# Kernel optimization log

Hardware: AMD Instinct MI355X
Metric: run time of the kernel (lower is better)

## Reference

```python
import jax, jax.numpy as jnp
import numpy as np

N = 100000
E = 1600000
D_IN = 128
D_OUT = 128
BN_EPS = 1e-5


def setup_inputs() -> dict:
    key = jax.random.key(0)
    k = jax.random.split(key, 8)
    feats = jax.random.normal(k[0], (N, D_IN), dtype=jnp.float32)
    src = jax.random.randint(k[1], (E,), 0, N, dtype=jnp.int32)
    dst = jax.random.randint(k[2], (E,), 0, N, dtype=jnp.int32)
    # GraphConv weight (in, out) + bias, residual Linear, batchnorm affine
    W = jax.random.normal(k[3], (D_IN, D_OUT), dtype=jnp.float32) / np.sqrt(D_IN)
    b = jnp.zeros((D_OUT,), dtype=jnp.float32)
    Wr = jax.random.normal(k[4], (D_IN, D_OUT), dtype=jnp.float32) / np.sqrt(D_IN)
    br = jnp.zeros((D_OUT,), dtype=jnp.float32)
    gamma = jnp.ones((D_OUT,), dtype=jnp.float32)
    beta = jnp.zeros((D_OUT,), dtype=jnp.float32)
    return {"feats": feats, "src": src, "dst": dst, "W": W, "b": b,
            "Wr": Wr, "br": br, "gamma": gamma, "beta": beta}


def reference(feats, src, dst, W, b, Wr, br, gamma, beta):
    ones = jnp.ones((src.shape[0],), dtype=feats.dtype)
    out_deg = jax.ops.segment_sum(ones, src, num_segments=N)
    in_deg = jax.ops.segment_sum(ones, dst, num_segments=N)
    norm_src = jax.lax.rsqrt(jnp.maximum(out_deg, 1.0))  # [N]
    norm_dst = jax.lax.rsqrt(jnp.maximum(in_deg, 1.0))   # [N]

    # GraphConv, norm='both' (in_feats == out_feats -> aggregate then matmul)
    h = feats * norm_src[:, None]
    agg = jax.ops.segment_sum(h[src], dst, num_segments=N)  # [N, D_IN]
    agg = agg * norm_dst[:, None]
    conv = jax.nn.relu(agg @ W + b)

    # residual linear + activation
    res = jax.nn.relu(feats @ Wr + br)
    y = conv + res  # dropout p=0 -> identity

    # BatchNorm1d (batch statistics, biased variance)
    mean = jnp.mean(y, axis=0)
    var = jnp.var(y, axis=0)
    y = (y - mean) * jax.lax.rsqrt(var + BN_EPS) * gamma + beta
    return y
```

## Files before the change

kernel.cpp:

```cpp
#include <hip/hip_runtime.h>

#define NN 100000
#define DD 128
#define EE 1600000
#define BN_EPS 1e-5f
#define NBLK 3125
#define NCH 2
#define CH 50000
#define CW (CH / 4)
#define NEB 64
#define EPB (EE / NEB)

using bf16x8 = __attribute__((ext_vector_type(8))) short;
using f32x4  = __attribute__((ext_vector_type(4))) float;

__device__ __forceinline__ unsigned short bf16r(float f) {
    unsigned u = __float_as_uint(f);
    u += 0x7FFF + ((u >> 16) & 1);
    return (unsigned short)(u >> 16);
}
__device__ __forceinline__ float bf2f(unsigned short h) {
    return __uint_as_float((unsigned)h << 16);
}

__global__ __launch_bounds__(1024) void hist_kernel(
    const int4* __restrict__ src4, const int4* __restrict__ dst4,
    unsigned short* __restrict__ outT, unsigned short* __restrict__ inT,
    unsigned char* __restrict__ lrank) {
    __shared__ unsigned outc[CW];
    __shared__ unsigned inc[CW];
    const int j = blockIdx.x & (NEB - 1);
    const int c = blockIdx.x >> 6;
    const int clo = c * CH;
    const int t = threadIdx.x;
    for (int i = t; i < CW; i += 1024) { outc[i] = 0; inc[i] = 0; }
    __syncthreads();
    const int base = j * (EPB / 4);
    for (int i = t; i < EPB / 4; i += 1024) {
        int4 s = src4[base + i];
        int4 d = dst4[base + i];
        int e = j * EPB + i * 4;
        unsigned sx = (unsigned)(s.x - clo);
        unsigned sy = (unsigned)(s.y - clo);
        unsigned sz = (unsigned)(s.z - clo);
        unsigned sw = (unsigned)(s.w - clo);
        if (sx < CH) atomicAdd(&outc[sx >> 2], 1u << ((sx & 3) * 8));
        if (sy < CH) atomicAdd(&outc[sy >> 2], 1u << ((sy & 3) * 8));
        if (sz < CH) atomicAdd(&outc[sz >> 2], 1u << ((sz & 3) * 8));
        if (sw < CH) atomicAdd(&outc[sw >> 2], 1u << ((sw & 3) * 8));
        unsigned dx = (unsigned)(d.x - clo);
        unsigned dy = (unsigned)(d.y - clo);
        unsigned dz = (unsigned)(d.z - clo);
        unsigned dw = (unsigned)(d.w - clo);
        if (dx < CH) { unsigned o = atomicAdd(&inc[dx >> 2], 1u << ((dx & 3) * 8)); lrank[e + 0] = (unsigned char)(o >> ((dx & 3) * 8)); }
        if (dy < CH) { unsigned o = atomicAdd(&inc[dy >> 2], 1u << ((dy & 3) * 8)); lrank[e + 1] = (unsigned char)(o >> ((dy & 3) * 8)); }
        if (dz < CH) { unsigned o = atomicAdd(&inc[dz >> 2], 1u << ((dz & 3) * 8)); lrank[e + 2] = (unsigned char)(o >> ((dz & 3) * 8)); }
        if (dw < CH) { unsigned o = atomicAdd(&inc[dw >> 2], 1u << ((dw & 3) * 8)); lrank[e + 3] = (unsigned char)(o >> ((dw & 3) * 8)); }
    }
    __syncthreads();
    ushort4* op = (ushort4*)(outT + (size_t)j * NN + clo);
    ushort4* ip = (ushort4*)(inT + (size_t)j * NN + clo);
    for (int i = t; i < CW; i += 1024) {
        unsigned vo = outc[i], vi = inc[i];
        ushort4 ho, hi;
        ho.x = (unsigned short)(vo & 0xFFu);
        ho.y = (unsigned short)((vo >> 8) & 0xFFu);
        ho.z = (unsigned short)((vo >> 16) & 0xFFu);
        ho.w = (unsigned short)(vo >> 24);
        hi.x = (unsigned short)(vi & 0xFFu);
        hi.y = (unsigned short)((vi >> 8) & 0xFFu);
        hi.z = (unsigned short)((vi >> 16) & 0xFFu);
        hi.w = (unsigned short)(vi >> 24);
        op[i] = ho;
        ip[i] = hi;
    }
}

__global__ void degscan_kernel(const unsigned short* __restrict__ outT,
                               unsigned short* __restrict__ inT,
                               int* __restrict__ indeg, float* __restrict__ ns,
                               float* __restrict__ nd) {
    int n = blockIdx.x * blockDim.x + threadIdx.x;
    if (n < NN) {
        int run_in = 0, run_out = 0;
#pragma unroll 8
        for (int j = 0; j < NEB; ++j) {
            run_out += (int)outT[(size_t)j * NN + n];
            int ci = (int)inT[(size_t)j * NN + n];
            inT[(size_t)j * NN + n] = (unsigned short)run_in;
            run_in += ci;
        }
        indeg[n] = run_in;
        ns[n] = rsqrtf(fmaxf((float)run_out, 1.0f));
        nd[n] = rsqrtf(fmaxf((float)run_in, 1.0f));
    }
}

__global__ __launch_bounds__(1024) void scan1_kernel(const int* __restrict__ indeg,
                                                     int* __restrict__ partial,
                                                     int* __restrict__ blocksum) {
    __shared__ int s[1024];
    int t = threadIdx.x;
    int idx = blockIdx.x * 1024 + t;
    int v = (idx < NN) ? indeg[idx] : 0;
    s[t] = v;
    __syncthreads();
    for (int off = 1; off < 1024; off <<= 1) {
        int x = (t >= off) ? s[t - off] : 0;
        __syncthreads();
        s[t] += x;
        __syncthreads();
    }
    if (idx < NN) partial[idx] = s[t] - v;
    if (t == 1023) blocksum[blockIdx.x] = s[t];
}

__global__ void scan23_kernel(const int* __restrict__ partial, const int* __restrict__ blocksum,
                              int* __restrict__ row_ofs) {
    __shared__ int s[128];
    int t = threadIdx.x;
    if (t < 128) s[t] = (t < 98) ? blocksum[t] : 0;
    __syncthreads();
    for (int off = 1; off < 128; off <<= 1) {
        int x = (t < 128 && t >= off) ? s[t - off] : 0;
        __syncthreads();
        if (t < 128) s[t] += x;
        __syncthreads();
    }
    int i = blockIdx.x * blockDim.x + t;
    if (i < NN) {
        int bk = i >> 10;
        row_ofs[i] = partial[i] + s[bk] - blocksum[bk];
        if (i == 0) row_ofs[NN] = EE;
    }
}

__global__ void fill4_kernel(const int4* __restrict__ src4, const int4* __restrict__ dst4,
                             const unsigned short* __restrict__ baseT,
                             const uchar4* __restrict__ lrank4,
                             const int* __restrict__ row_ofs, int* __restrict__ e_src) {
    int i = blockIdx.x * blockDim.x + threadIdx.x;
    if (i < EE / 4) {
        int4 s = src4[i];
        int4 d = dst4[i];
        uchar4 r = lrank4[i];
        int j = (i * 4) / EPB;
        const unsigned short* bT = baseT + (size_t)j * NN;
        e_src[row_ofs[d.x] + (int)bT[d.x] + (int)r.x] = s.x;
        e_src[row_ofs[d.y] + (int)bT[d.y] + (int)r.y] = s.y;
        e_src[row_ofs[d.z] + (int)bT[d.z] + (int)r.z] = s.z;
        e_src[row_ofs[d.w] + (int)bT[d.w] + (int)r.w] = s.w;
    }
}

__global__ void cvt_kernel(const float4* __restrict__ feats4, const float* __restrict__ ns,
                           ushort4* __restrict__ fb4) {
    int i = blockIdx.x * blockDim.x + threadIdx.x;
    if (i < NN * 32) {
        float s = ns[i >> 5];
        float4 v = feats4[i];
        ushort4 h;
        h.x = bf16r(v.x * s);
        h.y = bf16r(v.y * s);
        h.z = bf16r(v.z * s);
        h.w = bf16r(v.w * s);
        fb4[i] = h;
    }
}

__global__ void prepw_kernel(const float* __restrict__ W, const float* __restrict__ Wr,
                             unsigned short* __restrict__ wb) {
    int g = blockIdx.x >> 5;
    int f = blockIdx.x & 31;
    int ct = f >> 2, ks = f & 3;
    int l = threadIdx.x;
    const float* G = g ? Wr : W;
    unsigned short* hi = wb + (((size_t)(g * 2 + 0) * 32 + f) * 64 + l) * 8;
    unsigned short* lo = wb + (((size_t)(g * 2 + 1) * 32 + f) * 64 + l) * 8;
    for (int i = 0; i < 8; ++i) {
        int k = ks * 32 + (l >> 4) * 8 + i;
        int col = ct * 16 + (l & 15);
        float w = G[k * 128 + col];
        unsigned uh = __float_as_uint(w) & 0xFFFF0000u;
        hi[i] = (unsigned short)(uh >> 16);
        lo[i] = bf16r(w - __uint_as_float(uh));
    }
}

__device__ __forceinline__ void accum8(float* a, int4 u) {
    a[0] += __uint_as_float((unsigned)u.x << 16);
    a[1] += __uint_as_float((unsigned)u.x & 0xFFFF0000u);
    a[2] += __uint_as_float((unsigned)u.y << 16);
    a[3] += __uint_as_float((unsigned)u.y & 0xFFFF0000u);
    a[4] += __uint_as_float((unsigned)u.z << 16);
    a[5] += __uint_as_float((unsigned)u.z & 0xFFFF0000u);
    a[6] += __uint_as_float((unsigned)u.w << 16);
    a[7] += __uint_as_float((unsigned)u.w & 0xFFFF0000u);
}

__global__ __launch_bounds__(256, 6) void gather_kernel(
    const int4* __restrict__ fbi, const float* __restrict__ nd,
    const int* __restrict__ row_ofs, const int* __restrict__ e_src,
    float* __restrict__ y) {
    const int lane = threadIdx.x & 15;
    const int grp = threadIdx.x >> 4;
    const int node = blockIdx.x * 16 + grp;
    const int beg = row_ofs[node];
    const int end = row_ofs[node + 1];

    float a0[8] = {0.f, 0.f, 0.f, 0.f, 0.f, 0.f, 0.f, 0.f};
    float a1[8] = {0.f, 0.f, 0.f, 0.f, 0.f, 0.f, 0.f, 0.f};

    for (int e = beg; e < end; e += 16) {
        int cnt = end - e;
        if (cnt > 16) cnt = 16;
        int myidx = (lane < cnt) ? e_src[e + lane] : 0;
        int j = 0;
        for (; j + 3 < cnt; j += 4) {
            int s0 = __shfl(myidx, j, 16);
            int s1 = __shfl(myidx, j + 1, 16);
            int s2 = __shfl(myidx, j + 2, 16);
            int s3 = __shfl(myidx, j + 3, 16);
            int4 u0 = fbi[(size_t)s0 * 16 + lane];
            int4 u1 = fbi[(size_t)s1 * 16 + lane];
            int4 u2 = fbi[(size_t)s2 * 16 + lane];
            int4 u3 = fbi[(size_t)s3 * 16 + lane];
            accum8(a0, u0);
            accum8(a1, u1);
            accum8(a0, u2);
            accum8(a1, u3);
        }
        for (; j < cnt; ++j) {
            int s0 = __shfl(myidx, j, 16);
            int4 u0 = fbi[(size_t)s0 * 16 + lane];
            accum8(a0, u0);
        }
    }

    float snd = nd[node];
    float4 o0, o1;
    o0.x = (a0[0] + a1[0]) * snd;
    o0.y = (a0[1] + a1[1]) * snd;
    o0.z = (a0[2] + a1[2]) * snd;
    o0.w = (a0[3] + a1[3]) * snd;
    o1.x = (a0[4] + a1[4]) * snd;
    o1.y = (a0[5] + a1[5]) * snd;
    o1.z = (a0[6] + a1[6]) * snd;
    o1.w = (a0[7] + a1[7]) * snd;
    ((float4*)y)[(size_t)node * 32 + lane * 2] = o0;
    ((float4*)y)[(size_t)node * 32 + lane * 2 + 1] = o1;
}

__device__ __forceinline__ void hilo4(float4 v, ushort4& h, ushort4& l) {
    unsigned u0 = __float_as_uint(v.x) & 0xFFFF0000u;
    unsigned u1 = __float_as_uint(v.y) & 0xFFFF0000u;
    unsigned u2 = __float_as_uint(v.z) & 0xFFFF0000u;
    unsigned u3 = __float_as_uint(v.w) & 0xFFFF0000u;
    h.x = (unsigned short)(u0 >> 16);
    h.y = (unsigned short)(u1 >> 16);
    h.z = (unsigned short)(u2 >> 16);
    h.w = (unsigned short)(u3 >> 16);
    l.x = bf16r(v.x - __uint_as_float(u0));
    l.y = bf16r(v.y - __uint_as_float(u1));
    l.z = bf16r(v.z - __uint_as_float(u2));
    l.w = bf16r(v.w - __uint_as_float(u3));
}

__global__ __launch_bounds__(256, 4) void gemm_kernel(
    const float4* __restrict__ feats4,
    const unsigned short* __restrict__ wb,
    const float* __restrict__ b, const float* __restrict__ br,
    float* y, float* __restrict__ part_sum, float* __restrict__ part_sq) {
    __shared__ unsigned short AsH[32 * 128];
    __shared__ unsigned short AsL[32 * 128];
    __shared__ unsigned short FsH[32 * 128];
    __shared__ unsigned short FsL[32 * 128];

    const int tid = threadIdx.x;
    const int block_row = blockIdx.x * 32;
    const float4* agg4 = (const float4*)y;

    for (int i = tid; i < 1024; i += 256) {
        int r = i >> 5;
        int c4 = i & 31;
        size_t g = (size_t)(block_row + r) * 32 + c4;
        float4 a = agg4[g];
        float4 f = feats4[g];
        int off = (r * 256 + ((c4 * 8) ^ ((r & 7) << 4))) >> 1;
        ushort4 h, l;
        hilo4(a, h, l);
        *(ushort4*)(&AsH[off]) = h;
        *(ushort4*)(&AsL[off]) = l;
        hilo4(f, h, l);
        *(ushort4*)(&FsH[off]) = h;
        *(ushort4*)(&FsL[off]) = l;
    }
    __syncthreads();

    const int w = tid >> 6;
    const int l = tid & 63;
    const int lr = l & 15;
    const int lh = l >> 4;
    const int ct0 = w * 2;
    const bf16x8* WB = (const bf16x8*)wb;

    const f32x4 fzero = {0.f, 0.f, 0.f, 0.f};
    f32x4 aC[2][2], aR[2][2];
#pragma unroll
    for (int r = 0; r < 2; ++r)
#pragma unroll
        for (int c = 0; c < 2; ++c) { aC[r][c] = fzero; aR[r][c] = fzero; }

#pragma unroll 1
    for (int ks = 0; ks < 4; ++ks) {
        bf16x8 ah[2], al[2], fh[2], fl[2];
#pragma unroll
        for (int r = 0; r < 2; ++r) {
            int row = r * 16 + lr;
            int off = (row * 256 + ((ks * 64 + lh * 16) ^ ((row & 7) << 4))) >> 1;
            ah[r] = *(const bf16x8*)(&AsH[off]);
            al[r] = *(const bf16x8*)(&AsL[off]);
            fh[r] = *(const bf16x8*)(&FsH[off]);
            fl[r] = *(const bf16x8*)(&FsL[off]);
        }
#pragma unroll
        for (int c = 0; c < 2; ++c) {
            int fr = (ct0 + c) * 4 + ks;
            bf16x8 wh  = WB[(0 * 32 + fr) * 64 + l];
            bf16x8 wl  = WB[(1 * 32 + fr) * 64 + l];
            bf16x8 wrh = WB[(2 * 32 + fr) * 64 + l];
            bf16x8 wrl = WB[(3 * 32 + fr) * 64 + l];
#pragma unroll
            for (int r = 0; r < 2; ++r) {
                aC[r][c] = __builtin_amdgcn_mfma_f32_16x16x32_bf16(ah[r], wh, aC[r][c], 0, 0, 0);
                aC[r][c] = __builtin_amdgcn_mfma_f32_16x16x32_bf16(al[r], wh, aC[r][c], 0, 0, 0);
                aC[r][c] = __builtin_amdgcn_mfma_f32_16x16x32_bf16(ah[r], wl, aC[r][c], 0, 0, 0);
                aR[r][c] = __builtin_amdgcn_mfma_f32_16x16x32_bf16(fh[r], wrh, aR[r][c], 0, 0, 0);
                aR[r][c] = __builtin_amdgcn_mfma_f32_16x16x32_bf16(fl[r], wrh, aR[r][c], 0, 0, 0);
                aR[r][c] = __builtin_amdgcn_mfma_f32_16x16x32_bf16(fh[r], wrl, aR[r][c], 0, 0, 0);
            }
        }
    }

#pragma unroll
    for (int c = 0; c < 2; ++c) {
        int col = (ct0 + c) * 16 + lr;
        float bv = b[col], brv = br[col];
        float cs = 0.f, cq = 0.f;
#pragma unroll
        for (int r = 0; r < 2; ++r) {
#pragma unroll
            for (int i = 0; i < 4; ++i) {
                float o = fmaxf(aC[r][c][i] + bv, 0.f) + fmaxf(aR[r][c][i] + brv, 0.f);
                int grow = block_row + r * 16 + lh * 4 + i;
                y[(size_t)grow * 128 + col] = o;
                cs += o;
                cq += o * o;
            }
        }
        cs += __shfl_xor(cs, 16); cs += __shfl_xor(cs, 32);
        cq += __shfl_xor(cq, 16); cq += __shfl_xor(cq, 32);
        if (lh == 0) {
            part_sum[(size_t)blockIdx.x * 128 + col] = cs;
            part_sq[(size_t)blockIdx.x * 128 + col] = cq;
        }
    }
}

__global__ __launch_bounds__(256) void colreduce_kernel(
    const float* __restrict__ part_sum, const float* __restrict__ part_sq,
    float* __restrict__ colsum, float* __restrict__ colsumsq) {
    int j = blockIdx.x;
    int t = threadIdx.x;
    float s = 0.f, q = 0.f;
    for (int bb = t; bb < NBLK; bb += 256) {
        s += part_sum[(size_t)bb * 128 + j];
        q += part_sq[(size_t)bb * 128 + j];
    }
#pragma unroll
    for (int off = 1; off < 64; off <<= 1) {
        s += __shfl_xor(s, off);
        q += __shfl_xor(q, off);
    }
    __shared__ float ss[4], qq[4];
    if ((t & 63) == 0) { ss[t >> 6] = s; qq[t >> 6] = q; }
    __syncthreads();
    if (t == 0) {
        colsum[j] = ss[0] + ss[1] + ss[2] + ss[3];
        colsumsq[j] = qq[0] + qq[1] + qq[2] + qq[3];
    }
}

__global__ void apply2_kernel(float4* __restrict__ y4,
                              const float* __restrict__ colsum, const float* __restrict__ colsumsq,
                              const float* __restrict__ gamma, const float* __restrict__ beta) {
    __shared__ float sc4[128], sh4[128];
    int t = threadIdx.x;
    if (t < 128) {
        const float inv_n = 1.0f / (float)NN;
        float mean = colsum[t] * inv_n;
        float var = colsumsq[t] * inv_n - mean * mean;
        float s = gamma[t] * rsqrtf(var + BN_EPS);
        sc4[t] = s;
        sh4[t] = beta[t] - mean * s;
    }
    __syncthreads();
    int i = blockIdx.x * 256 + t;
    if (i < NN * 32) {
        int c = (i & 31) * 4;
        float4 v = y4[i];
        v.x = v.x * sc4[c + 0] + sh4[c + 0];
        v.y = v.y * sc4[c + 1] + sh4[c + 1];
        v.z = v.z * sc4[c + 2] + sh4[c + 2];
        v.w = v.w * sc4[c + 3] + sh4[c + 3];
        y4[i] = v;
    }
}

extern "C" void kernel_launch(void* const* d_in, const int* in_sizes, int n_in,
                              void* d_out, int out_size, void* d_ws, size_t ws_size,
                              hipStream_t stream) {
    const float* feats = (const float*)d_in[0];
    const int* src = (const int*)d_in[1];
    const int* dst = (const int*)d_in[2];
    const float* W = (const float*)d_in[3];
    const float* b = (const float*)d_in[4];
    const float* Wr = (const float*)d_in[5];
    const float* br = (const float*)d_in[6];
    const float* gamma = (const float*)d_in[7];
    const float* beta = (const float*)d_in[8];
    float* y = (float*)d_out;

    char* ws = (char*)d_ws;
    unsigned short* outT = (unsigned short*)ws;
    unsigned short* inT = outT + (size_t)NEB * NN;
    unsigned char* lrank = (unsigned char*)(inT + (size_t)NEB * NN);
    ushort4* fb4 = (ushort4*)ws;
    float* part_sum = (float*)lrank;
    float* part_sq = part_sum + (size_t)NBLK * 128;
    char* wsB = ws + (size_t)2 * NEB * NN * 2 + (size_t)EE * 2;
    float* ns = (float*)wsB;
    float* nd = ns + NN;
    int* row_ofs = (int*)(nd + NN);
    int* indeg = row_ofs + NN + 1;
    int* partial = indeg + NN;
    int* blocksum = partial + NN;
    int* e_src = blocksum + 128;
    float* colsum = (float*)(e_src + EE);
    float* colsumsq = colsum + DD;
    unsigned long long wbofs = (unsigned long long)((char*)(colsumsq + DD) - ws);
    wbofs = (wbofs + 255ull) & ~255ull;
    unsigned short* wb = (unsigned short*)(ws + wbofs);

    prepw_kernel<<<64, 64, 0, stream>>>(W, Wr, wb);
    hist_kernel<<<NCH * NEB, 1024, 0, stream>>>((const int4*)src, (const int4*)dst,
                                                outT, inT, lrank);
    degscan_kernel<<<(NN + 255) / 256, 256, 0, stream>>>(outT, inT, indeg, ns, nd);
    scan1_kernel<<<98, 1024, 0, stream>>>(indeg, partial, blocksum);
    scan23_kernel<<<(NN + 255) / 256, 256, 0, stream>>>(partial, blocksum, row_ofs);
    fill4_kernel<<<(EE / 4 + 255) / 256, 256, 0, stream>>>((const int4*)src, (const int4*)dst,
                                                           inT, (const uchar4*)lrank,
                                                           row_ofs, e_src);
    cvt_kernel<<<(NN * 32 + 255) / 256, 256, 0, stream>>>((const float4*)feats, ns, fb4);
    gather_kernel<<<NN / 16, 256, 0, stream>>>((const int4*)fb4, nd, row_ofs, e_src, y);
    gemm_kernel<<<NBLK, 256, 0, stream>>>((const float4*)feats, wb, b, br,
                                          y, part_sum, part_sq);
    colreduce_kernel<<<128, 256, 0, stream>>>(part_sum, part_sq, colsum, colsumsq);
    apply2_kernel<<<(NN * 32 + 255) / 256, 256, 0, stream>>>((float4*)y, colsum, colsumsq,
                                                             gamma, beta);
}
```

Baseline: 315.7 us.

## Shrink degree tables to bytes, fuse degree scan into scan1, unroll gather by 8

The per-edge-block histogram tables and the per-block in-degree prefix tables now use 8-bit entries instead of 16-bit, halving their write and read traffic in hist, scan and fill. The separate degscan kernel is folded into scan1, which now computes per-node degrees, norms and the block prefix in one pass. This drops a launch and the indeg round trip, but only 98 blocks of 1024 threads now do the 64 strided loads per node. The gather inner loop gains an 8-way unrolled path to keep more row loads in flight. The 8-bit prefix assumes each node's in-degree stays below 256.

```diff
diff --git a/kernel.cpp b/kernel.cpp
--- a/kernel.cpp
+++ b/kernel.cpp
@@ -25,7 +25,7 @@
 
 __global__ __launch_bounds__(1024) void hist_kernel(
     const int4* __restrict__ src4, const int4* __restrict__ dst4,
-    unsigned short* __restrict__ outT, unsigned short* __restrict__ inT,
+    unsigned char* __restrict__ outT8, unsigned char* __restrict__ inT8,
     unsigned char* __restrict__ lrank) {
     __shared__ unsigned outc[CW];
     __shared__ unsigned inc[CW];
@@ -58,51 +58,35 @@
         if (dw < CH) { unsigned o = atomicAdd(&inc[dw >> 2], 1u << ((dw & 3) * 8)); lrank[e + 3] = (unsigned char)(o >> ((dw & 3) * 8)); }
     }
     __syncthreads();
-    ushort4* op = (ushort4*)(outT + (size_t)j * NN + clo);
-    ushort4* ip = (ushort4*)(inT + (size_t)j * NN + clo);
+    unsigned* op = (unsigned*)(outT8 + (size_t)j * NN + clo);
+    unsigned* ip = (unsigned*)(inT8 + (size_t)j * NN + clo);
     for (int i = t; i < CW; i += 1024) {
-        unsigned vo = outc[i], vi = inc[i];
-        ushort4 ho, hi;
-        ho.x = (unsigned short)(vo & 0xFFu);
-        ho.y = (unsigned short)((vo >> 8) & 0xFFu);
-        ho.z = (unsigned short)((vo >> 16) & 0xFFu);
-        ho.w = (unsigned short)(vo >> 24);
-        hi.x = (unsigned short)(vi & 0xFFu);
-        hi.y = (unsigned short)((vi >> 8) & 0xFFu);
-        hi.z = (unsigned short)((vi >> 16) & 0xFFu);
-        hi.w = (unsigned short)(vi >> 24);
-        op[i] = ho;
-        ip[i] = hi;
-    }
-}
-
-__global__ void degscan_kernel(const unsigned short* __restrict__ outT,
-                               unsigned short* __restrict__ inT,
-                               int* __restrict__ indeg, float* __restrict__ ns,
-                               float* __restrict__ nd) {
-    int n = blockIdx.x * blockDim.x + threadIdx.x;
-    if (n < NN) {
-        int run_in = 0, run_out = 0;
-#pragma unroll 8
-        for (int j = 0; j < NEB; ++j) {
-            run_out += (int)outT[(size_t)j * NN + n];
-            int ci = (int)inT[(size_t)j * NN + n];
-            inT[(size_t)j * NN + n] = (unsigned short)run_in;
-            run_in += ci;
-        }
-        indeg[n] = run_in;
-        ns[n] = rsqrtf(fmaxf((float)run_out, 1.0f));
-        nd[n] = rsqrtf(fmaxf((float)run_in, 1.0f));
-    }
-}
-
-__global__ __launch_bounds__(1024) void scan1_kernel(const int* __restrict__ indeg,
-                                                     int* __restrict__ partial,
-                                                     int* __restrict__ blocksum) {
+        op[i] = outc[i];
+        ip[i] = inc[i];
+    }
+}
+
+__global__ __launch_bounds__(1024) void scan1_kernel(
+    const unsigned char* __restrict__ outT8, unsigned char* __restrict__ inT8,
+    int* __restrict__ partial, int* __restrict__ blocksum,
+    float* __restrict__ ns, float* __restrict__ nd) {
     __shared__ int s[1024];
     int t = threadIdx.x;
     int idx = blockIdx.x * 1024 + t;
-    int v = (idx < NN) ? indeg[idx] : 0;
+    int run_in = 0;
+    if (idx < NN) {
+        int run_out = 0;
+#pragma unroll 8
+        for (int j = 0; j < NEB; ++j) {
+            run_out += (int)outT8[(size_t)j * NN + idx];
+            int ci = (int)inT8[(size_t)j * NN + idx];
+            inT8[(size_t)j * NN + idx] = (unsigned char)run_in;
+            run_in += ci;
+        }
+        ns[idx] = rsqrtf(fmaxf((float)run_out, 1.0f));
+        nd[idx] = rsqrtf(fmaxf((float)run_in, 1.0f));
+    }
+    int v = run_in;
     s[t] = v;
     __syncthreads();
     for (int off = 1; off < 1024; off <<= 1) {
@@ -136,7 +120,7 @@
 }
 
 __global__ void fill4_kernel(const int4* __restrict__ src4, const int4* __restrict__ dst4,
-                             const unsigned short* __restrict__ baseT,
+                             const unsigned char* __restrict__ baseT8,
                              const uchar4* __restrict__ lrank4,
                              const int* __restrict__ row_ofs, int* __restrict__ e_src) {
     int i = blockIdx.x * blockDim.x + threadIdx.x;
@@ -145,7 +129,7 @@
         int4 d = dst4[i];
         uchar4 r = lrank4[i];
         int j = (i * 4) / EPB;
-        const unsigned short* bT = baseT + (size_t)j * NN;
+        const unsigned char* bT = baseT8 + (size_t)j * NN;
         e_src[row_ofs[d.x] + (int)bT[d.x] + (int)r.x] = s.x;
         e_src[row_ofs[d.y] + (int)bT[d.y] + (int)r.y] = s.y;
         e_src[row_ofs[d.z] + (int)bT[d.z] + (int)r.z] = s.z;
@@ -216,6 +200,32 @@
         if (cnt > 16) cnt = 16;
         int myidx = (lane < cnt) ? e_src[e + lane] : 0;
         int j = 0;
+        for (; j + 7 < cnt; j += 8) {
+            int s0 = __shfl(myidx, j, 16);
+            int s1 = __shfl(myidx, j + 1, 16);
+            int s2 = __shfl(myidx, j + 2, 16);
+            int s3 = __shfl(myidx, j + 3, 16);
+            int s4 = __shfl(myidx, j + 4, 16);
+            int s5 = __shfl(myidx, j + 5, 16);
+            int s6 = __shfl(myidx, j + 6, 16);
+            int s7 = __shfl(myidx, j + 7, 16);
+            int4 u0 = fbi[(size_t)s0 * 16 + lane];
+            int4 u1 = fbi[(size_t)s1 * 16 + lane];
+            int4 u2 = fbi[(size_t)s2 * 16 + lane];
+            int4 u3 = fbi[(size_t)s3 * 16 + lane];
+            int4 u4 = fbi[(size_t)s4 * 16 + lane];
+            int4 u5 = fbi[(size_t)s5 * 16 + lane];
+            int4 u6 = fbi[(size_t)s6 * 16 + lane];
+            int4 u7 = fbi[(size_t)s7 * 16 + lane];
+            accum8(a0, u0);
+            accum8(a1, u1);
+            accum8(a0, u2);
+            accum8(a1, u3);
+            accum8(a0, u4);
+            accum8(a1, u5);
+            accum8(a0, u6);
+            accum8(a1, u7);
+        }
         for (; j + 3 < cnt; j += 4) {
             int s0 = __shfl(myidx, j, 16);
             int s1 = __shfl(myidx, j + 1, 16);
@@ -432,18 +442,17 @@
     float* y = (float*)d_out;
 
     char* ws = (char*)d_ws;
-    unsigned short* outT = (unsigned short*)ws;
-    unsigned short* inT = outT + (size_t)NEB * NN;
-    unsigned char* lrank = (unsigned char*)(inT + (size_t)NEB * NN);
+    unsigned char* outT8 = (unsigned char*)ws;
+    unsigned char* inT8 = outT8 + (size_t)NEB * NN;
+    unsigned char* lrank = inT8 + (size_t)NEB * NN;
     ushort4* fb4 = (ushort4*)ws;
     float* part_sum = (float*)lrank;
     float* part_sq = part_sum + (size_t)NBLK * 128;
-    char* wsB = ws + (size_t)2 * NEB * NN * 2 + (size_t)EE * 2;
+    char* wsB = ws + (size_t)NN * 32 * 8;
     float* ns = (float*)wsB;
     float* nd = ns + NN;
     int* row_ofs = (int*)(nd + NN);
-    int* indeg = row_ofs + NN + 1;
-    int* partial = indeg + NN;
+    int* partial = row_ofs + NN + 1;
     int* blocksum = partial + NN;
     int* e_src = blocksum + 128;
     float* colsum = (float*)(e_src + EE);
@@ -454,12 +463,11 @@
 
     prepw_kernel<<<64, 64, 0, stream>>>(W, Wr, wb);
     hist_kernel<<<NCH * NEB, 1024, 0, stream>>>((const int4*)src, (const int4*)dst,
-                                                outT, inT, lrank);
-    degscan_kernel<<<(NN + 255) / 256, 256, 0, stream>>>(outT, inT, indeg, ns, nd);
-    scan1_kernel<<<98, 1024, 0, stream>>>(indeg, partial, blocksum);
+                                                outT8, inT8, lrank);
+    scan1_kernel<<<98, 1024, 0, stream>>>(outT8, inT8, partial, blocksum, ns, nd);
     scan23_kernel<<<(NN + 255) / 256, 256, 0, stream>>>(partial, blocksum, row_ofs);
     fill4_kernel<<<(EE / 4 + 255) / 256, 256, 0, stream>>>((const int4*)src, (const int4*)dst,
-                                                           inT, (const uchar4*)lrank,
+                                                           inT8, (const uchar4*)lrank,
                                                            row_ofs, e_src);
     cvt_kernel<<<(NN * 32 + 255) / 256, 256, 0, stream>>>((const float4*)feats, ns, fb4);
     gather_kernel<<<NN / 16, 256, 0, stream>>>((const int4*)fb4, nd, row_ofs, e_src, y);
```

Result: faster. 308.6 us (-2.2%).
